# Kernel tuning notes

Measured on AMD Instinct MI355X. Metric: run time of the kernel, lower is better.

## Reference

```python
import jax, jax.numpy as jnp
import numpy as np
from jax import lax

COUNT_W, DM_W, OT_W = 3.0, 0.5, 0.3
SL1_BETA = 10.0
DM_SIGMA, DM_DS = 8.0, 4
OT_REG, OT_ITERS, OT_DS = 0.1, 50, 8
EPS = 1e-8


def _gauss_kernel(sigma):
    size = int(6 * sigma) | 1  # 49
    x = np.arange(size, dtype=np.float32) - size // 2
    xx, yy = np.meshgrid(x, x)
    k = np.exp(-(xx ** 2 + yy ** 2) / (2 * sigma ** 2))
    k = k / k.sum()
    return jnp.asarray(k, jnp.float32)[None, None], size // 2  # [1,1,S,S], pad


def _block_sum(x, d):
    # avg_pool2d(kernel=d) * d^2 == block sum
    B, C, H, W = x.shape
    return x.reshape(B, C, H // d, d, W // d, d).sum(axis=(3, 5))


def _cost_matrix(H, W):
    y, x = jnp.meshgrid(jnp.arange(H, dtype=jnp.float32),
                        jnp.arange(W, dtype=jnp.float32), indexing='ij')
    coords = jnp.stack([y.ravel(), x.ravel()], axis=1)  # [N,2]
    d = coords[:, None, :] - coords[None, :, :]
    return (d ** 2).sum(-1)  # [N,N] squared euclidean


def _dm_loss(pred, gt):
    p = _block_sum(pred, DM_DS)
    g = _block_sum(gt, DM_DS)
    kern, pad = _gauss_kernel(DM_SIGMA)
    conv = lambda z: lax.conv_general_dilated(
        z, kern, (1, 1), [(pad, pad), (pad, pad)],
        dimension_numbers=('NCHW', 'OIHW', 'NCHW'))
    ps, gs = conv(p), conv(g)
    pn = ps / jnp.maximum(ps.sum(axis=(2, 3), keepdims=True), EPS)
    gn = gs / jnp.maximum(gs.sum(axis=(2, 3), keepdims=True), EPS)
    kl = (gn * jnp.log((gn + EPS) / (pn + EPS))).sum(axis=(2, 3))
    l2 = ((pn - gn) ** 2).sum(axis=(2, 3))
    return kl.mean() + l2.mean()


def _ot_loss(pred, gt):
    p = _block_sum(pred, OT_DS)  # [B,1,h,w]
    g = _block_sum(gt, OT_DS)
    B, _, h, w = p.shape
    N = h * w
    a_raw = p.reshape(B, N)
    b_raw = g.reshape(B, N)
    a_sum = jnp.maximum(a_raw.sum(-1), EPS)
    b_sum = jnp.maximum(b_raw.sum(-1), EPS)
    a = a_raw / a_sum[:, None]
    b = b_raw / b_sum[:, None]
    C = _cost_matrix(h, w)          # [N,N]
    K = jnp.exp(-C / OT_REG)        # [N,N]

    def step(uv, _):
        u, _v = uv
        v = b / (u @ K + EPS)       # K.T @ u, batched
        u = a / (v @ K.T + EPS)     # K @ v, batched
        return (u, v), None

    (u, v), _ = lax.scan(step, (jnp.ones_like(a), jnp.ones_like(b)),
                         None, length=OT_ITERS)
    cost = jnp.einsum('bn,nm,bm->b', u, K * C, v)  # sum(P*C), P=diag(u)K diag(v)
    mask = (a_sum > 0.5) & (b_sum > 0.5)
    return jnp.where(mask, cost, 0.0).sum() / B


def reference(pred_density, gt_density, gt_counts, cell_area):
    B = pred_density.shape[0]
    # count loss (smooth L1, beta=10)
    pred_counts = jnp.maximum(pred_density.sum(axis=(1, 2, 3)) / cell_area, 0.0)
    gt_counts_f = gt_counts.astype(jnp.float32)
    diff = jnp.abs(pred_counts - gt_counts_f)
    count_loss = jnp.where(diff < SL1_BETA,
                           0.5 * diff ** 2 / SL1_BETA,
                           diff - 0.5 * SL1_BETA).mean()
    dm = _dm_loss(pred_density, gt_density)
    ot = _ot_loss(pred_density, gt_density)
    return COUNT_W * count_loss + DM_W * dm + OT_W * ot


def setup_inputs() -> dict:
    key = jax.random.key(0)
    k1, k2, k3 = jax.random.split(key, 3)
    B, H, W = 16, 512, 512
    return {
        'pred_density': jax.random.uniform(k1, (B, 1, H, W), jnp.float32),
        'gt_density': jax.random.uniform(k2, (B, 1, H, W), jnp.float32),
        'gt_counts': jax.random.randint(k3, (B,), 0, 500, jnp.int32),
        'cell_area': 1,
    }
```

## Files before the change

kernel.cpp:

```cpp
#include <hip/hip_runtime.h>
#include <math.h>

constexpr int B   = 16;
constexpr int H   = 512, W = 512;
constexpr int HW  = H * W;
constexpr int P4  = 128;
constexpr int P4N = P4 * P4;
constexpr int P8N = 64 * 64;
constexpr int NIMG = 2 * B;

constexpr float KW1 = 4.5399929762484854e-05f;
constexpr float KC2 = 4.1223072448771156e-09f;

constexpr size_t OFF_P4   = 0;
constexpr size_t OFF_CV   = OFF_P4  + (size_t)NIMG * P4N;
constexpr size_t OFF_P8   = OFF_CV  + (size_t)NIMG * P4N;
constexpr size_t OFF_PART = OFF_P8  + (size_t)NIMG * P8N;
constexpr size_t OFF_CSUM = OFF_PART + 512;

__device__ __forceinline__ float dpp_up(float x) {
    return __int_as_float(__builtin_amdgcn_update_dpp(
        0, __float_as_int(x), 0x138, 0xf, 0xf, true));
}
__device__ __forceinline__ float dpp_dn(float x) {
    return __int_as_float(__builtin_amdgcn_update_dpp(
        0, __float_as_int(x), 0x130, 0xf, 0xf, true));
}

__global__ void k_pre8(const float* __restrict__ pred, const float* __restrict__ gt,
                       float* __restrict__ ws, float* __restrict__ out, int out_size) {
    int tid = threadIdx.x, bx = blockIdx.x;
    if (bx == 0) {
        for (int i = tid; i < out_size; i += 256) out[i] = 0.f;
    }
    int gid = bx * 256 + tid;
    int img = gid >> 12;
    int rem = gid & (P8N - 1);
    int y = rem >> 6, x = rem & 63;
    const float* src = (img < B) ? (pred + (size_t)img * HW)
                                 : (gt + (size_t)(img - B) * HW);
    const float4* s4 = reinterpret_cast<const float4*>(src);
    int base = y * 8 * 128 + x * 2;
    float q00 = 0.f, q01 = 0.f, q10 = 0.f, q11 = 0.f;
#pragma unroll
    for (int r = 0; r < 8; r++) {
        float4 a0 = s4[base + r * 128];
        float4 a1 = s4[base + r * 128 + 1];
        float sa = a0.x + a0.y + a0.z + a0.w;
        float sb = a1.x + a1.y + a1.z + a1.w;
        if (r < 4) { q00 += sa; q01 += sb; } else { q10 += sa; q11 += sb; }
    }
    float* p4 = ws + OFF_P4 + (size_t)img * P4N;
    p4[(2 * y) * 128 + 2 * x]         = q00;
    p4[(2 * y) * 128 + 2 * x + 1]     = q01;
    p4[(2 * y + 1) * 128 + 2 * x]     = q10;
    p4[(2 * y + 1) * 128 + 2 * x + 1] = q11;
    float s8 = q00 + q01 + q10 + q11;
    ws[OFF_P8 + gid] = s8;
    float part = s8;
#pragma unroll
    for (int o = 32; o > 0; o >>= 1) part += __shfl_down(part, o, 64);
    __shared__ float r4[4];
    int lane = tid & 63, wid = tid >> 6;
    if (lane == 0) r4[wid] = part;
    __syncthreads();
    if (tid == 0) ws[OFF_PART + bx] = r4[0] + r4[1] + r4[2] + r4[3];
}

__global__ void __launch_bounds__(512) k_mega(float* __restrict__ ws,
                                              const int* __restrict__ gtc,
                                              const int* __restrict__ carea,
                                              float* __restrict__ out) {
    __shared__ float sh[P4N + 80];
    int tid = threadIdx.x;
    int lane = tid & 63, w = tid >> 6;

    if (blockIdx.x < 32) {
        int img = blockIdx.x;
        float* hbuf = sh;
        float* wlds = sh + P4N;
        float* rs   = sh + P4N + 56;
        if (tid < 49) {
            float xx = (float)(tid - 24);
            wlds[tid] = expf(-xx * xx * (1.f / 128.f));
        }
        __syncthreads();
        float norm = 0.f;
#pragma unroll
        for (int k = 0; k < 49; k++) norm += wlds[k];
        float inv = 1.f / norm;
        const float* src = ws + OFF_P4 + (size_t)img * P4N;

#pragma unroll
        for (int g = 0; g < 4; g++) {
            int unit = g * 512 + tid;
            int r = unit >> 4, seg = unit & 15, x0 = seg * 8;
            const float4* row4 = reinterpret_cast<const float4*>(src + (size_t)r * 128);
            float v[56];
#pragma unroll
            for (int j = 0; j < 14; j++) {
                int fx = (x0 - 24) / 4 + j;
                float4 t = (fx >= 0 && fx < 32) ? row4[fx] : make_float4(0.f, 0.f, 0.f, 0.f);
                v[4 * j] = t.x; v[4 * j + 1] = t.y; v[4 * j + 2] = t.z; v[4 * j + 3] = t.w;
            }
            float o8[8];
#pragma unroll
            for (int i = 0; i < 8; i++) o8[i] = 0.f;
#pragma unroll
            for (int k = 0; k < 49; k++) {
                float wk = wlds[k];
#pragma unroll
                for (int i = 0; i < 8; i++) o8[i] = fmaf(wk, v[i + k], o8[i]);
            }
            int sw = r & 31;
#pragma unroll
            for (int i = 0; i < 8; i++)
                hbuf[r * 128 + ((x0 + i) ^ sw)] = o8[i] * inv;
        }
        __syncthreads();

        float part = 0.f;
        float* dst = ws + OFF_CV + (size_t)img * P4N;
#pragma unroll
        for (int g = 0; g < 4; g++) {
            int unit = g * 512 + tid;
            int c = unit & 127, rseg = unit >> 7, r0 = rseg * 8;
            float v[56];
#pragma unroll
            for (int j = 0; j < 56; j++) {
                int rr = r0 - 24 + j;
                v[j] = (rr >= 0 && rr < 128) ? hbuf[rr * 128 + (c ^ (rr & 31))] : 0.f;
            }
            float o8[8];
#pragma unroll
            for (int i = 0; i < 8; i++) o8[i] = 0.f;
#pragma unroll
            for (int k = 0; k < 49; k++) {
                float wk = wlds[k];
#pragma unroll
                for (int i = 0; i < 8; i++) o8[i] = fmaf(wk, v[i + k], o8[i]);
            }
#pragma unroll
            for (int i = 0; i < 8; i++) {
                float s = o8[i] * inv;
                dst[(size_t)(r0 + i) * 128 + c] = s;
                part += s;
            }
        }
#pragma unroll
        for (int o = 32; o > 0; o >>= 1) part += __shfl_down(part, o, 64);
        if (lane == 0) rs[w] = part;
        __syncthreads();
        if (tid == 0) {
            float s = 0.f;
#pragma unroll
            for (int i = 0; i < 8; i++) s += rs[i];
            ws[OFF_CSUM + img] = s;
        }
    } else {
        int b = blockIdx.x - 32;
        int r0 = w << 3;
        float* H0 = sh;
        float* H1 = sh + 2048;
        float* rsum = sh + 4096;

        const float* PART = ws + OFF_PART;
        float rawA = 0.f, rawB = 0.f;
#pragma unroll
        for (int j = 0; j < 16; j++) {
            rawA += PART[b * 16 + j];
            rawB += PART[(B + b) * 16 + j];
        }
        float asum = fmaxf(rawA, 1e-8f), bsum = fmaxf(rawB, 1e-8f);
        float ai = 1.f / asum, bi = 1.f / bsum;
        const float* ap = ws + OFF_P8 + (size_t)b * P8N;
        const float* bp = ws + OFF_P8 + (size_t)(B + b) * P8N;

        float ar[8], br10[10], cur[8], vr[10];
#pragma unroll
        for (int k = 0; k < 8; k++) {
            ar[k] = ap[(r0 + k) * 64 + lane] * ai;
            cur[k] = 1.f;
        }
#pragma unroll
        for (int i = 0; i < 10; i++) {
            int rr = r0 - 1 + i;
            br10[i] = (rr >= 0 && rr < 64) ? bp[rr * 64 + lane] * bi : 0.f;
        }

        for (int it = 0; it < 50; it++) {
            float* Hp = (it & 1) ? H1 : H0;
            Hp[(0 * 8 + w) * 64 + lane] = cur[0];
            Hp[(1 * 8 + w) * 64 + lane] = cur[1];
            Hp[(2 * 8 + w) * 64 + lane] = cur[6];
            Hp[(3 * 8 + w) * 64 + lane] = cur[7];
            __syncthreads();
            float uext[12];
            uext[0]  = w ? Hp[(2 * 8 + w - 1) * 64 + lane] : 0.f;
            uext[1]  = w ? Hp[(3 * 8 + w - 1) * 64 + lane] : 0.f;
#pragma unroll
            for (int k = 0; k < 8; k++) uext[2 + k] = cur[k];
            uext[10] = (w < 7) ? Hp[(0 * 8 + w + 1) * 64 + lane] : 0.f;
            uext[11] = (w < 7) ? Hp[(1 * 8 + w + 1) * 64 + lane] : 0.f;

            float tr[10];
#pragma unroll
            for (int i = 0; i < 10; i++)
                tr[i] = fmaf(KW1, uext[i] + uext[i + 2], uext[i + 1]);
#pragma unroll
            for (int i = 0; i < 10; i++) {
                float s = fmaf(KW1, dpp_up(tr[i]) + dpp_dn(tr[i]), tr[i]) + 1e-8f;
                vr[i] = br10[i] * __builtin_amdgcn_rcpf(s);
            }
            float t2[8];
#pragma unroll
            for (int k = 0; k < 8; k++)
                t2[k] = fmaf(KW1, vr[k] + vr[k + 2], vr[k + 1]);
#pragma unroll
            for (int k = 0; k < 8; k++) {
                float s = fmaf(KW1, dpp_up(t2[k]) + dpp_dn(t2[k]), t2[k]) + 1e-8f;
                cur[k] = ar[k] * __builtin_amdgcn_rcpf(s);
            }
        }

        float dL[10], dR[10];
#pragma unroll
        for (int i = 0; i < 10; i++) { dL[i] = dpp_up(vr[i]); dR[i] = dpp_dn(vr[i]); }
        float part = 0.f;
#pragma unroll
        for (int k = 0; k < 8; k++) {
            float s = KW1 * (vr[k] + vr[k + 2] + dL[k + 1] + dR[k + 1])
                    + KC2 * (dL[k] + dR[k] + dL[k + 2] + dR[k + 2]);
            part = fmaf(cur[k], s, part);
        }
#pragma unroll
        for (int o = 32; o > 0; o >>= 1) part += __shfl_down(part, o, 64);
        if (lane == 0) rsum[w] = part;
        __syncthreads();
        if (tid == 0) {
            float c = 0.f;
#pragma unroll
            for (int i = 0; i < 8; i++) c += rsum[i];
            float ot = (asum > 0.5f && bsum > 0.5f) ? c : 0.f;
            int cv = carea[0];
            float ca = (cv >= 1 && cv < 16777216) ? (float)cv : __int_as_float(cv);
            float pc = fmaxf(rawA / ca, 0.f);
            float d = fabsf(pc - (float)gtc[b]);
            float cl = (d < 10.f) ? (0.05f * d * d) : (d - 5.f);
            atomicAdd(out, 0.3f * ot * (1.f / 16.f) + 3.f * cl * (1.f / 16.f));
        }
    }
}

__global__ void k_kll2(const float* __restrict__ ws, float* __restrict__ out) {
    int idx = blockIdx.x * 256 + threadIdx.x;
    int b = idx >> 12, rem = idx & 4095;
    const float4* cv4 = reinterpret_cast<const float4*>(ws + OFF_CV);
    float4 p = cv4[(size_t)b * 4096 + rem];
    float4 g = cv4[(size_t)(B + b) * 4096 + rem];
    float isp = 1.f / fmaxf(ws[OFF_CSUM + b], 1e-8f);
    float isg = 1.f / fmaxf(ws[OFF_CSUM + B + b], 1e-8f);
    float part = 0.f;
#pragma unroll
    for (int j = 0; j < 4; j++) {
        float pn = (j == 0 ? p.x : j == 1 ? p.y : j == 2 ? p.z : p.w) * isp;
        float gn = (j == 0 ? g.x : j == 1 ? g.y : j == 2 ? g.z : g.w) * isg;
        float d = pn - gn;
        part += gn * __logf((gn + 1e-8f) / (pn + 1e-8f)) + d * d;
    }
#pragma unroll
    for (int o = 32; o > 0; o >>= 1) part += __shfl_down(part, o, 64);
    __shared__ float r4[4];
    int lane = threadIdx.x & 63, wid = threadIdx.x >> 6;
    if (lane == 0) r4[wid] = part;
    __syncthreads();
    if (threadIdx.x == 0)
        atomicAdd(out, (0.5f / 16.f) * (r4[0] + r4[1] + r4[2] + r4[3]));
}

extern "C" void kernel_launch(void* const* d_in, const int* in_sizes, int n_in,
                              void* d_out, int out_size, void* d_ws, size_t ws_size,
                              hipStream_t stream) {
    const float* pred = (const float*)d_in[0];
    const float* gt   = (const float*)d_in[1];
    const int* gtc    = (const int*)d_in[2];
    const int* ca     = (const int*)d_in[3];
    float* out = (float*)d_out;
    float* ws  = (float*)d_ws;

    k_pre8<<<512, 256, 0, stream>>>(pred, gt, ws, out, out_size);
    k_mega<<<48, 512, 0, stream>>>(ws, gtc, ca, out);
    k_kll2<<<256, 256, 0, stream>>>(ws, out);
}
```

Before: 123.8 us.

## Fuse KL/L2 reduction into conv blocks, one block per batch pair

Each conv block now handles both the pred and gt image of one batch element in sequence, holding the blurred results in registers. It then computes the KL and L2 terms directly, which removes the conv output buffer, the per-image sum buffer and the separate reduction kernel launch. The p4 stores are also vectorised to float2. In exchange, the conv work runs on 16 blocks instead of 32, so each block does twice the serial work. Register pressure also rises from 64 held values per thread under a launch-bounds hint of 2 blocks per CU, which could lengthen the critical path.

```diff
diff --git a/kernel.cpp b/kernel.cpp
--- a/kernel.cpp
+++ b/kernel.cpp
@@ -13,10 +13,8 @@
 constexpr float KC2 = 4.1223072448771156e-09f;
 
 constexpr size_t OFF_P4   = 0;
-constexpr size_t OFF_CV   = OFF_P4  + (size_t)NIMG * P4N;
-constexpr size_t OFF_P8   = OFF_CV  + (size_t)NIMG * P4N;
+constexpr size_t OFF_P8   = OFF_P4  + (size_t)NIMG * P4N;
 constexpr size_t OFF_PART = OFF_P8  + (size_t)NIMG * P8N;
-constexpr size_t OFF_CSUM = OFF_PART + 512;
 
 __device__ __forceinline__ float dpp_up(float x) {
     return __int_as_float(__builtin_amdgcn_update_dpp(
@@ -50,11 +48,9 @@
         float sb = a1.x + a1.y + a1.z + a1.w;
         if (r < 4) { q00 += sa; q01 += sb; } else { q10 += sa; q11 += sb; }
     }
-    float* p4 = ws + OFF_P4 + (size_t)img * P4N;
-    p4[(2 * y) * 128 + 2 * x]         = q00;
-    p4[(2 * y) * 128 + 2 * x + 1]     = q01;
-    p4[(2 * y + 1) * 128 + 2 * x]     = q10;
-    p4[(2 * y + 1) * 128 + 2 * x + 1] = q11;
+    float2* p42 = reinterpret_cast<float2*>(ws + OFF_P4 + (size_t)img * P4N);
+    p42[(2 * y) * 64 + x]     = make_float2(q00, q01);
+    p42[(2 * y + 1) * 64 + x] = make_float2(q10, q11);
     float s8 = q00 + q01 + q10 + q11;
     ws[OFF_P8 + gid] = s8;
     float part = s8;
@@ -67,19 +63,89 @@
     if (tid == 0) ws[OFF_PART + bx] = r4[0] + r4[1] + r4[2] + r4[3];
 }
 
-__global__ void __launch_bounds__(512) k_mega(float* __restrict__ ws,
-                                              const int* __restrict__ gtc,
-                                              const int* __restrict__ carea,
-                                              float* __restrict__ out) {
-    __shared__ float sh[P4N + 80];
+__device__ __forceinline__ float conv_pass(const float* __restrict__ src, float inv,
+                                           const float* __restrict__ wlds,
+                                           float* __restrict__ hbuf,
+                                           float* __restrict__ rs,
+                                           float* __restrict__ cvreg, int tid) {
+#pragma unroll
+    for (int g = 0; g < 4; g++) {
+        int unit = g * 512 + tid;
+        int r = unit >> 4, seg = unit & 15, x0 = seg * 8;
+        const float4* row4 = reinterpret_cast<const float4*>(src + (size_t)r * 128);
+        float v[56];
+#pragma unroll
+        for (int j = 0; j < 14; j++) {
+            int fx = (x0 - 24) / 4 + j;
+            float4 t = (fx >= 0 && fx < 32) ? row4[fx] : make_float4(0.f, 0.f, 0.f, 0.f);
+            v[4 * j] = t.x; v[4 * j + 1] = t.y; v[4 * j + 2] = t.z; v[4 * j + 3] = t.w;
+        }
+        float o8[8];
+#pragma unroll
+        for (int i = 0; i < 8; i++) o8[i] = 0.f;
+#pragma unroll
+        for (int k = 0; k < 49; k++) {
+            float wk = wlds[k];
+#pragma unroll
+            for (int i = 0; i < 8; i++) o8[i] = fmaf(wk, v[i + k], o8[i]);
+        }
+        int sw = r & 31;
+#pragma unroll
+        for (int i = 0; i < 8; i++)
+            hbuf[r * 128 + ((x0 + i) ^ sw)] = o8[i] * inv;
+    }
+    __syncthreads();
+
+    float part = 0.f;
+#pragma unroll
+    for (int g = 0; g < 4; g++) {
+        int unit = g * 512 + tid;
+        int c = unit & 127, rseg = unit >> 7, r0 = rseg * 8;
+        float v[56];
+#pragma unroll
+        for (int j = 0; j < 56; j++) {
+            int rr = r0 - 24 + j;
+            v[j] = (rr >= 0 && rr < 128) ? hbuf[rr * 128 + (c ^ (rr & 31))] : 0.f;
+        }
+        float o8[8];
+#pragma unroll
+        for (int i = 0; i < 8; i++) o8[i] = 0.f;
+#pragma unroll
+        for (int k = 0; k < 49; k++) {
+            float wk = wlds[k];
+#pragma unroll
+            for (int i = 0; i < 8; i++) o8[i] = fmaf(wk, v[i + k], o8[i]);
+        }
+#pragma unroll
+        for (int i = 0; i < 8; i++) {
+            float s = o8[i] * inv;
+            cvreg[g * 8 + i] = s;
+            part += s;
+        }
+    }
+#pragma unroll
+    for (int o = 32; o > 0; o >>= 1) part += __shfl_down(part, o, 64);
+    int lane = tid & 63, w = tid >> 6;
+    if (lane == 0) rs[w] = part;
+    __syncthreads();
+    float tot = 0.f;
+#pragma unroll
+    for (int i = 0; i < 8; i++) tot += rs[i];
+    return tot;
+}
+
+__global__ void __launch_bounds__(512, 2) k_mega(float* __restrict__ ws,
+                                                 const int* __restrict__ gtc,
+                                                 const int* __restrict__ carea,
+                                                 float* __restrict__ out) {
+    __shared__ float hbuf[P4N];
+    __shared__ float wlds[49];
+    __shared__ float rs[8];
     int tid = threadIdx.x;
     int lane = tid & 63, w = tid >> 6;
 
-    if (blockIdx.x < 32) {
-        int img = blockIdx.x;
-        float* hbuf = sh;
-        float* wlds = sh + P4N;
-        float* rs   = sh + P4N + 56;
+    if (blockIdx.x < 16) {
+        int b = blockIdx.x;
         if (tid < 49) {
             float xx = (float)(tid - 24);
             wlds[tid] = expf(-xx * xx * (1.f / 128.f));
@@ -89,63 +155,21 @@
 #pragma unroll
         for (int k = 0; k < 49; k++) norm += wlds[k];
         float inv = 1.f / norm;
-        const float* src = ws + OFF_P4 + (size_t)img * P4N;
-
-#pragma unroll
-        for (int g = 0; g < 4; g++) {
-            int unit = g * 512 + tid;
-            int r = unit >> 4, seg = unit & 15, x0 = seg * 8;
-            const float4* row4 = reinterpret_cast<const float4*>(src + (size_t)r * 128);
-            float v[56];
-#pragma unroll
-            for (int j = 0; j < 14; j++) {
-                int fx = (x0 - 24) / 4 + j;
-                float4 t = (fx >= 0 && fx < 32) ? row4[fx] : make_float4(0.f, 0.f, 0.f, 0.f);
-                v[4 * j] = t.x; v[4 * j + 1] = t.y; v[4 * j + 2] = t.z; v[4 * j + 3] = t.w;
-            }
-            float o8[8];
-#pragma unroll
-            for (int i = 0; i < 8; i++) o8[i] = 0.f;
-#pragma unroll
-            for (int k = 0; k < 49; k++) {
-                float wk = wlds[k];
-#pragma unroll
-                for (int i = 0; i < 8; i++) o8[i] = fmaf(wk, v[i + k], o8[i]);
-            }
-            int sw = r & 31;
-#pragma unroll
-            for (int i = 0; i < 8; i++)
-                hbuf[r * 128 + ((x0 + i) ^ sw)] = o8[i] * inv;
-        }
-        __syncthreads();
-
+
+        float cv_p[32], cv_g[32];
+        float sum_p = conv_pass(ws + OFF_P4 + (size_t)b * P4N, inv, wlds, hbuf, rs,
+                                cv_p, tid);
+        float sum_g = conv_pass(ws + OFF_P4 + (size_t)(B + b) * P4N, inv, wlds, hbuf,
+                                rs, cv_g, tid);
+
+        float isp = 1.f / fmaxf(sum_p, 1e-8f);
+        float isg = 1.f / fmaxf(sum_g, 1e-8f);
         float part = 0.f;
-        float* dst = ws + OFF_CV + (size_t)img * P4N;
-#pragma unroll
-        for (int g = 0; g < 4; g++) {
-            int unit = g * 512 + tid;
-            int c = unit & 127, rseg = unit >> 7, r0 = rseg * 8;
-            float v[56];
-#pragma unroll
-            for (int j = 0; j < 56; j++) {
-                int rr = r0 - 24 + j;
-                v[j] = (rr >= 0 && rr < 128) ? hbuf[rr * 128 + (c ^ (rr & 31))] : 0.f;
-            }
-            float o8[8];
-#pragma unroll
-            for (int i = 0; i < 8; i++) o8[i] = 0.f;
-#pragma unroll
-            for (int k = 0; k < 49; k++) {
-                float wk = wlds[k];
-#pragma unroll
-                for (int i = 0; i < 8; i++) o8[i] = fmaf(wk, v[i + k], o8[i]);
-            }
-#pragma unroll
-            for (int i = 0; i < 8; i++) {
-                float s = o8[i] * inv;
-                dst[(size_t)(r0 + i) * 128 + c] = s;
-                part += s;
-            }
+#pragma unroll
+        for (int j = 0; j < 32; j++) {
+            float pn = cv_p[j] * isp, gn = cv_g[j] * isg;
+            float d = pn - gn;
+            part += gn * __logf((gn + 1e-8f) / (pn + 1e-8f)) + d * d;
         }
 #pragma unroll
         for (int o = 32; o > 0; o >>= 1) part += __shfl_down(part, o, 64);
@@ -155,14 +179,13 @@
             float s = 0.f;
 #pragma unroll
             for (int i = 0; i < 8; i++) s += rs[i];
-            ws[OFF_CSUM + img] = s;
+            atomicAdd(out, (0.5f / 16.f) * s);
         }
     } else {
-        int b = blockIdx.x - 32;
+        int b = blockIdx.x - 16;
         int r0 = w << 3;
-        float* H0 = sh;
-        float* H1 = sh + 2048;
-        float* rsum = sh + 4096;
+        float* H0 = hbuf;
+        float* H1 = hbuf + 2048;
 
         const float* PART = ws + OFF_PART;
         float rawA = 0.f, rawB = 0.f;
@@ -235,12 +258,12 @@
         }
 #pragma unroll
         for (int o = 32; o > 0; o >>= 1) part += __shfl_down(part, o, 64);
-        if (lane == 0) rsum[w] = part;
+        if (lane == 0) rs[w] = part;
         __syncthreads();
         if (tid == 0) {
             float c = 0.f;
 #pragma unroll
-            for (int i = 0; i < 8; i++) c += rsum[i];
+            for (int i = 0; i < 8; i++) c += rs[i];
             float ot = (asum > 0.5f && bsum > 0.5f) ? c : 0.f;
             int cv = carea[0];
             float ca = (cv >= 1 && cv < 16777216) ? (float)cv : __int_as_float(cv);
@@ -250,32 +273,6 @@
             atomicAdd(out, 0.3f * ot * (1.f / 16.f) + 3.f * cl * (1.f / 16.f));
         }
     }
-}
-
-__global__ void k_kll2(const float* __restrict__ ws, float* __restrict__ out) {
-    int idx = blockIdx.x * 256 + threadIdx.x;
-    int b = idx >> 12, rem = idx & 4095;
-    const float4* cv4 = reinterpret_cast<const float4*>(ws + OFF_CV);
-    float4 p = cv4[(size_t)b * 4096 + rem];
-    float4 g = cv4[(size_t)(B + b) * 4096 + rem];
-    float isp = 1.f / fmaxf(ws[OFF_CSUM + b], 1e-8f);
-    float isg = 1.f / fmaxf(ws[OFF_CSUM + B + b], 1e-8f);
-    float part = 0.f;
-#pragma unroll
-    for (int j = 0; j < 4; j++) {
-        float pn = (j == 0 ? p.x : j == 1 ? p.y : j == 2 ? p.z : p.w) * isp;
-        float gn = (j == 0 ? g.x : j == 1 ? g.y : j == 2 ? g.z : g.w) * isg;
-        float d = pn - gn;
-        part += gn * __logf((gn + 1e-8f) / (pn + 1e-8f)) + d * d;
-    }
-#pragma unroll
-    for (int o = 32; o > 0; o >>= 1) part += __shfl_down(part, o, 64);
-    __shared__ float r4[4];
-    int lane = threadIdx.x & 63, wid = threadIdx.x >> 6;
-    if (lane == 0) r4[wid] = part;
-    __syncthreads();
-    if (threadIdx.x == 0)
-        atomicAdd(out, (0.5f / 16.f) * (r4[0] + r4[1] + r4[2] + r4[3]));
 }
 
 extern "C" void kernel_launch(void* const* d_in, const int* in_sizes, int n_in,
@@ -289,6 +286,5 @@
     float* ws  = (float*)d_ws;
 
     k_pre8<<<512, 256, 0, stream>>>(pred, gt, ws, out, out_size);
-    k_mega<<<48, 512, 0, stream>>>(ws, gtc, ca, out);
-    k_kll2<<<256, 256, 0, stream>>>(ws, out);
-}
+    k_mega<<<32, 512, 0, stream>>>(ws, gtc, ca, out);
+}
```

Measured after the change: 256.5 us. +107.2%, slower.
